# Optimization experiments

Measured on AMD Instinct MI355X. Metric: run time of the kernel, lower is better.

## Reference

```python
import jax, jax.numpy as jnp
import numpy as np

B, S, E, H = 4, 1024, 1024, 16
HD = E // H
EPS = 1e-10


def setup_inputs() -> dict:
    key = jax.random.key(0)
    ks = jax.random.split(key, 10)
    w = lambda k: jax.random.normal(k, (E, E), jnp.float32) * 0.02
    b = lambda k: jax.random.normal(k, (E,), jnp.float32) * 0.02
    return {
        "query": jax.random.normal(ks[0], (B, S, E), jnp.float32),
        "Wq": w(ks[1]), "bq": b(ks[2]),
        "Wk": w(ks[3]), "bk": b(ks[4]),
        "Wv": w(ks[5]), "bv": b(ks[6]),
        "Wo": w(ks[7]), "bo": b(ks[8]),
        "alpha": jnp.array(1.0, jnp.float32),
    }


def reference(query, Wq, bq, Wk, bk, Wv, bv, Wo, bo, alpha):
    scale = 1.0 / np.sqrt(HD)
    # projections -> [B, H, S, HD]
    def heads(x, W, bias):
        return (x @ W.T + bias).reshape(B, S, H, HD).transpose(0, 2, 1, 3)
    Q = heads(query, Wq, bq)
    K = heads(query, Wk, bk)
    V = heads(query, Wv, bv)
    # raw scores [B, H, S, S]
    scores = jnp.einsum('bhqd,bhkd->bhqk', Q, K) * scale
    # 2D FFT over the (q, k) plane
    scores_fft = jnp.fft.fft2(scores, axes=(-2, -1))
    # spectral filter: exp(i * alpha * arctan(log|F| + eps))
    phase = alpha * jnp.arctan(jnp.log(jnp.abs(scores_fft) + EPS))
    filt = jnp.exp(1j * phase)
    scores_filtered = jnp.fft.ifft2(scores_fft * filt, axes=(-2, -1)).real
    # softmax over keys (dropout is identity at eval)
    attn = jax.nn.softmax(scores_filtered, axis=-1)
    ctx = jnp.einsum('bhqk,bhkd->bhqd', attn, V)
    ctx = ctx.transpose(0, 2, 1, 3).reshape(B, S, E)
    return ctx @ Wo.T + bo
```

## Files before the change

kernel.cpp:

```cpp
#include <hip/hip_runtime.h>
#include <hip/hip_fp16.h>


typedef __attribute__((ext_vector_type(8))) short short8;
typedef __attribute__((ext_vector_type(8))) _Float16 half8;
typedef __attribute__((ext_vector_type(4))) float f32x4;

#define PITCH 40
#define PITCH1 72
#define TP 40

__device__ __forceinline__ float bf2f(short v) {
  return __uint_as_float(((unsigned)(unsigned short)v) << 16);
}
__device__ __forceinline__ short f2bf(float f) {
  unsigned u = __float_as_uint(f);
  u += 0x7FFFu + ((u >> 16) & 1u);
  return (short)(u >> 16);
}

__device__ __forceinline__ short8 ld8(const void* p, size_t idx, int isf32) {
  short8 r;
  if (isf32) {
    const float* f = (const float*)p + idx;
    float4 a = *(const float4*)f;
    float4 b = *(const float4*)(f + 4);
    r[0] = f2bf(a.x); r[1] = f2bf(a.y); r[2] = f2bf(a.z); r[3] = f2bf(a.w);
    r[4] = f2bf(b.x); r[5] = f2bf(b.y); r[6] = f2bf(b.z); r[7] = f2bf(b.w);
  } else {
    r = *(const short8*)((const short*)p + idx);
  }
  return r;
}
__device__ __forceinline__ float ldf(const void* p, int idx, int isf32) {
  return isf32 ? ((const float*)p)[idx] : bf2f(((const short*)p)[idx]);
}

__device__ __forceinline__ float2 cmul(float2 a, float2 b) {
  return make_float2(a.x * b.x - a.y * b.y, a.x * b.y + a.y * b.x);
}
__device__ __forceinline__ float2 cadd(float2 a, float2 b) {
  return make_float2(a.x + b.x, a.y + b.y);
}
__device__ __forceinline__ float2 csub(float2 a, float2 b) {
  return make_float2(a.x - b.x, a.y - b.y);
}
__device__ __forceinline__ half8 hneg(half8 v) {
  int4 t = *(int4*)&v;
  t.x ^= 0x80008000; t.y ^= 0x80008000; t.z ^= 0x80008000; t.w ^= 0x80008000;
  return *(half8*)&t;
}


template <int SGN>
__device__ __forceinline__ void dft16_dif(float2* x) {
  const float C16[8] = {1.f, 0.92387953f, 0.70710678f, 0.38268343f,
                        0.f, -0.38268343f, -0.70710678f, -0.92387953f};
  const float S16[8] = {0.f, 0.38268343f, 0.70710678f, 0.92387953f,
                        1.f, 0.92387953f, 0.70710678f, 0.38268343f};
#pragma unroll
  for (int h = 8; h >= 1; h >>= 1)
#pragma unroll
    for (int b = 0; b < 16; b += 2 * h)
#pragma unroll
      for (int i = 0; i < h; ++i) {
        const int e = i * (8 / h);
        float2 u = x[b + i], v = x[b + i + h];
        x[b + i] = cadd(u, v);
        float2 d = csub(u, v);
        float2 w = make_float2(C16[e], SGN > 0 ? S16[e] : -S16[e]);
        x[b + i + h] = (e == 0) ? d : cmul(d, w);
      }
}

template <int SGN>
__device__ __forceinline__ void midtw(float2* x, int lane) {
  const int rho[16] = {0, 8, 4, 12, 2, 10, 6, 14, 1, 9, 5, 13, 3, 11, 7, 15};
  float s, c;
  __sincosf((float)lane * 0.00613592315f, &s, &c);
  float2 w = make_float2(c, SGN > 0 ? s : -s);
  float2 run = w;
  x[8] = cmul(x[8], run);
#pragma unroll
  for (int e = 2; e < 16; ++e) {
    run = cmul(run, w);
    x[rho[e]] = cmul(x[rho[e]], run);
  }
}

template <int SGN>
__device__ __forceinline__ void xlane_dif(float2* x, int lane) {
#pragma unroll
  for (int h = 32; h >= 1; h >>= 1) {
    const int e = (lane & (h - 1)) * (32 / h);
    float s, c;
    __sincosf((float)e * 0.09817477042f, &s, &c);
    float2 w = make_float2(c, SGN > 0 ? s : -s);
    const bool hi = (lane & h) != 0;
#pragma unroll
    for (int r = 0; r < 16; ++r) {
      float2 t = x[r];
      float2 p;
      p.x = __shfl_xor(t.x, h, 64);
      p.y = __shfl_xor(t.y, h, 64);
      x[r] = hi ? cmul(csub(p, t), w) : cadd(t, p);
    }
  }
}

template <int SGN>
__device__ __forceinline__ void wfft1024_dif(float2* x, int lane) {
  dft16_dif<SGN>(x);
  midtw<SGN>(x, lane);
  xlane_dif<SGN>(x, lane);
}

template <int SGN>
__device__ __forceinline__ void midtw2(float2* x, float2* y, int lane) {
  const int rho[16] = {0, 8, 4, 12, 2, 10, 6, 14, 1, 9, 5, 13, 3, 11, 7, 15};
  float s, c;
  __sincosf((float)lane * 0.00613592315f, &s, &c);
  float2 w = make_float2(c, SGN > 0 ? s : -s);
  float2 run = w;
  x[8] = cmul(x[8], run);
  y[8] = cmul(y[8], run);
#pragma unroll
  for (int e = 2; e < 16; ++e) {
    run = cmul(run, w);
    x[rho[e]] = cmul(x[rho[e]], run);
    y[rho[e]] = cmul(y[rho[e]], run);
  }
}

template <int SGN>
__device__ __forceinline__ void xlane_dif2(float2* x, float2* y, int lane) {
#pragma unroll
  for (int h = 32; h >= 1; h >>= 1) {
    const int e = (lane & (h - 1)) * (32 / h);
    float s, c;
    __sincosf((float)e * 0.09817477042f, &s, &c);
    float2 w = make_float2(c, SGN > 0 ? s : -s);
    const bool hi = (lane & h) != 0;
#pragma unroll
    for (int r = 0; r < 16; ++r) {
      float2 t = x[r];
      float2 p;
      p.x = __shfl_xor(t.x, h, 64);
      p.y = __shfl_xor(t.y, h, 64);
      x[r] = hi ? cmul(csub(p, t), w) : cadd(t, p);
    }
#pragma unroll
    for (int r = 0; r < 16; ++r) {
      float2 t = y[r];
      float2 p;
      p.x = __shfl_xor(t.x, h, 64);
      p.y = __shfl_xor(t.y, h, 64);
      y[r] = hi ? cmul(csub(p, t), w) : cadd(t, p);
    }
  }
}

template <int SGN>
__device__ __forceinline__ void wfft1024_dif2(float2* x, float2* y, int lane) {
  dft16_dif<SGN>(x);
  dft16_dif<SGN>(y);
  midtw2<SGN>(x, y, lane);
  xlane_dif2<SGN>(x, y, lane);
}

__device__ __forceinline__ float gainw(float re, float im, float alpha, bool a1) {
  float mag2 = re * re + im * im;
  float t = 0.5f * __logf(mag2 + 1e-20f);
  if (a1) return __builtin_amdgcn_rsqf(fmaf(t, t, 1.0f)) * (1.0f / 1048576.0f);
  return __cosf(alpha * atanf(t)) * (1.0f / 1048576.0f);
}

__global__ void k0_detect(const unsigned* __restrict__ q,
                          const void* __restrict__ alphap, int* __restrict__ flags) {
  __shared__ float smax[256];
  __shared__ int szero[256];
  int t = threadIdx.x;
  float mx = 0.f; int zc = 0;
  for (int i = t; i < 16384; i += 256) {
    unsigned w = q[i];
    unsigned lo = w & 0xFFFFu;
    float v = fabsf(__uint_as_float(lo << 16));
    if (!(v <= 1e30f)) v = 1e30f;
    mx = fmaxf(mx, v);
    zc += (lo == 0u);
  }
  smax[t] = mx; szero[t] = zc;
  __syncthreads();
  for (int s = 128; s > 0; s >>= 1) {
    if (t < s) { smax[t] = fmaxf(smax[t], smax[t + s]); szero[t] += szero[t + s]; }
    __syncthreads();
  }
  if (t == 0) {
    int isf32 = (smax[0] > 100.f) || (szero[0] > 12288);
    flags[0] = isf32;
    float alpha = isf32 ? *(const float*)alphap : bf2f(*(const short*)alphap);
    ((float*)flags)[1] = alpha;
  }
}

__global__ __launch_bounds__(256) void k1_qkv(
    const void* __restrict__ x,
    const void* __restrict__ Wq, const void* __restrict__ bq,
    const void* __restrict__ Wk, const void* __restrict__ bk,
    const void* __restrict__ Wv, const void* __restrict__ bv,
    short* __restrict__ Qt, short* __restrict__ Kt, short* __restrict__ Vt,
    const int* __restrict__ flags)
{
  __shared__ __align__(16) char smem[128 * PITCH1 * 2 * 2];
  short* As = (short*)smem;
  short* Bs = As + 128 * PITCH1;
  short* Ct = (short*)smem;
  const int isf32 = flags[0];
  const int t = threadIdx.x;
  const int lb = blockIdx.x;
  const int m0 = ((lb & 7) * 4 + ((lb >> 3) & 3)) * 128;
  const int n0 = (lb >> 5) * 128;
  const int which = blockIdx.y;
  const void* __restrict__ W = (which == 0) ? Wq : (which == 1) ? Wk : Wv;
  const void* __restrict__ bias = (which == 0) ? bq : (which == 1) ? bk : bv;
  const int lane = t & 63, wvi = t >> 6;
  const int wr = wvi >> 1, wc = wvi & 1;
  const int lm = lane & 15, lq = lane >> 4;
  f32x4 acc[4][4] = {};

  for (int k0 = 0; k0 < 1024; k0 += 64) {
    __syncthreads();
#pragma unroll
    for (int i = 0; i < 4; ++i) {
      int l = t + i * 256;
      int row = l >> 3, kk = (l & 7) << 3;
      *(short8*)&As[row * PITCH1 + kk] = ld8(x, (size_t)(m0 + row) * 1024 + k0 + kk, isf32);
      *(short8*)&Bs[row * PITCH1 + kk] = ld8(W, (size_t)(n0 + row) * 1024 + k0 + kk, isf32);
    }
    __syncthreads();
#pragma unroll
    for (int kh = 0; kh < 2; ++kh) {
      short8 af[4], bf[4];
#pragma unroll
      for (int a = 0; a < 4; ++a)
        af[a] = *(const short8*)&As[(wr * 64 + a * 16 + lm) * PITCH1 + kh * 32 + lq * 8];
#pragma unroll
      for (int b = 0; b < 4; ++b)
        bf[b] = *(const short8*)&Bs[(wc * 64 + b * 16 + lm) * PITCH1 + kh * 32 + lq * 8];
#pragma unroll
      for (int a = 0; a < 4; ++a)
#pragma unroll
        for (int b = 0; b < 4; ++b)
          acc[a][b] = __builtin_amdgcn_mfma_f32_16x16x32_bf16(af[a], bf[b], acc[a][b], 0, 0, 0);
    }
  }

  __syncthreads();
#pragma unroll
  for (int a = 0; a < 4; ++a)
#pragma unroll
    for (int b = 0; b < 4; ++b) {
      int col = wc * 64 + b * 16 + lm;
      float bv_ = ldf(bias, n0 + col, isf32);
#pragma unroll
      for (int r = 0; r < 4; ++r) {
        int row = wr * 64 + a * 16 + lq * 4 + r;
        Ct[row * 136 + col] = f2bf(acc[a][b][r] + bv_);
      }
    }
  __syncthreads();

  short* __restrict__ O = (which == 0) ? Qt : (which == 1) ? Kt : Vt;
#pragma unroll
  for (int j = 0; j < 8; ++j) {
    int id = t + j * 256;
    int d128 = id & 127, sg = (id >> 7) * 8;
    short vals[8];
#pragma unroll
    for (int i = 0; i < 8; ++i) vals[i] = Ct[(sg + i) * 136 + d128];
    int col = n0 + d128;
    int h = col >> 6, d = col & 63;
    int bb = m0 >> 10, sbase = (m0 & 1023) + sg;
    *(short8*)&O[(((size_t)(bb * 16 + h)) << 16) + ((size_t)d << 10) + sbase] = *(short8*)vals;
  }
}

__global__ __launch_bounds__(128) void kA_qkfft(
    const short* __restrict__ Qt, const short* __restrict__ Kt,
    __half2* __restrict__ Qhat, __half2* __restrict__ Khat)
{
  __shared__ float2 sbuf[2][1024];
  const int lane = threadIdx.x & 63, w = threadIdx.x >> 6;
  const int z = blockIdx.y;
  const int bx = blockIdx.x;
  if (bx < 16) {
    const short* qp = Qt + ((size_t)z << 16);
    const int d0 = bx * 4 + w * 2;
    float2 x[16], y[16];
#pragma unroll
    for (int j = 0; j < 16; ++j) {
      x[j] = make_float2(0.125f * bf2f(qp[(d0 << 10) + lane + 64 * j]), 0.f);
      y[j] = make_float2(0.125f * bf2f(qp[((d0 + 1) << 10) + lane + 64 * j]), 0.f);
    }
    wfft1024_dif2<-1>(x, y, lane);
    __half2* o0 = Qhat + (((size_t)(z * 64 + d0)) << 10);
    __half2* o1 = o0 + 1024;
#pragma unroll
    for (int r = 0; r < 16; ++r) {
      o0[lane + 64 * r] = __float22half2_rn(x[r]);
      o1[lane + 64 * r] = __float22half2_rn(y[r]);
    }
  } else {
    const short* kp = Kt + ((size_t)z << 16);
    const int p = (bx - 16) * 2 + w;
    const int d0 = 2 * p;
    float2 x[16];
#pragma unroll
    for (int j = 0; j < 16; ++j)
      x[j] = make_float2(bf2f(kp[(d0 << 10) + lane + 64 * j]),
                         bf2f(kp[((d0 + 1) << 10) + lane + 64 * j]));
    wfft1024_dif<-1>(x, lane);
    const int rho[16] = {0, 8, 4, 12, 2, 10, 6, 14, 1, 9, 5, 13, 3, 11, 7, 15};
    const int bl6 = ((lane & 1) << 5) | ((lane & 2) << 3) | ((lane & 4) << 1) |
                    ((lane & 8) >> 1) | ((lane & 16) >> 3) | ((lane & 32) >> 5);
    float2* buf = sbuf[w];
#pragma unroll
    for (int r = 0; r < 16; ++r) buf[rho[r] + 16 * bl6] = x[r];
    __half2* o0 = Khat + (size_t)(z * 64 + d0) * 520;
    __half2* o1 = o0 + 520;
#pragma unroll 1
    for (int jj = 0; jj < 9; ++jj) {
      int v = lane + 64 * jj;
      if (v <= 512) {
        float2 A = buf[v], B = buf[(1024 - v) & 1023];
        o0[v] = __float22half2_rn(make_float2((A.x + B.x) * 0.5f, (A.y - B.y) * 0.5f));
        o1[v] = __float22half2_rn(make_float2((A.y + B.y) * 0.5f, (B.x - A.x) * 0.5f));
      }
    }
  }
}

__global__ __launch_bounds__(256) void kB_specmm(
    const __half2* __restrict__ Qhat, const __half2* __restrict__ Khat,
    __half2* __restrict__ Ct, const int* __restrict__ flags, int bh0)
{
  __shared__ unsigned short Are[64][72], Aim[64][72], Bre[128][72], Bim[128][72];
  const int t = threadIdx.x;
  const int u0 = blockIdx.x * 128;
  const int v0 = blockIdx.y * 64;
  const int zl = blockIdx.z;
  const int z = bh0 + zl;
  const float alpha = ((const float*)flags)[1];
  const bool a1 = (alpha == 1.0f);
  {
    const int d = t >> 2;
    const ushort2* src = (const ushort2*)(Khat + (size_t)(z * 64 + d) * 520);
    int vb = (t & 3) * 16;
#pragma unroll
    for (int j = 0; j < 16; ++j) {
      int v = v0 + vb + j;
      if (v > 519) v = 519;
      ushort2 e = src[v];
      int row = vb + j;
      int dc = d ^ (((row >> 4) & 3) << 4);
      Are[row][dc] = e.x;
      Aim[row][dc] = e.y;
    }
    const ushort2* srcb = (const ushort2*)(Qhat + (((size_t)(z * 64 + d)) << 10) + u0);
    int ub = (t & 3) * 32;
#pragma unroll
    for (int j = 0; j < 32; ++j) {
      ushort2 e = srcb[ub + j];
      int row = ub + j;
      int dc = d ^ (((row >> 5) & 3) << 4);
      Bre[row][dc] = e.x;
      Bim[row][dc] = e.y;
    }
  }
  __syncthreads();

  const int lane = t & 63, wc = t >> 6;
  const int lm = lane & 15, lq = lane >> 4;
  f32x4 cre[4][2] = {}, cim[4][2] = {};
#pragma unroll
  for (int ks = 0; ks < 2; ++ks) {
    half8 ar[4], ai[4], aiN[4], br[2], bi[2];
#pragma unroll
    for (int a = 0; a < 4; ++a) {
      int dc = (ks * 32 + lq * 8) ^ ((a & 3) << 4);
      ar[a] = *(const half8*)&Are[a * 16 + lm][dc];
      ai[a] = *(const half8*)&Aim[a * 16 + lm][dc];
      aiN[a] = hneg(ai[a]);
    }
#pragma unroll
    for (int n = 0; n < 2; ++n) {
      int dc = (ks * 32 + lq * 8) ^ ((wc & 3) << 4);
      br[n] = *(const half8*)&Bre[wc * 32 + n * 16 + lm][dc];
      bi[n] = *(const half8*)&Bim[wc * 32 + n * 16 + lm][dc];
    }
#pragma unroll
    for (int a = 0; a < 4; ++a)
#pragma unroll
      for (int n = 0; n < 2; ++n) {
        cre[a][n] = __builtin_amdgcn_mfma_f32_16x16x32_f16(ar[a], br[n], cre[a][n], 0, 0, 0);
        cre[a][n] = __builtin_amdgcn_mfma_f32_16x16x32_f16(aiN[a], bi[n], cre[a][n], 0, 0, 0);
        cim[a][n] = __builtin_amdgcn_mfma_f32_16x16x32_f16(ar[a], bi[n], cim[a][n], 0, 0, 0);
        cim[a][n] = __builtin_amdgcn_mfma_f32_16x16x32_f16(ai[a], br[n], cim[a][n], 0, 0, 0);
      }
  }

  __half2* outp = Ct + (size_t)zl * 513 * 1024 + u0 + wc * 32;
#pragma unroll
  for (int a = 0; a < 4; ++a)
#pragma unroll
    for (int r = 0; r < 4; ++r) {
      int v = v0 + a * 16 + lq * 4 + r;
      if (v < 513) {
#pragma unroll
        for (int n = 0; n < 2; ++n) {
          float re = cre[a][n][r], im = cim[a][n][r];
          float wf = gainw(re, im, alpha, a1);
          outp[(size_t)v * 1024 + n * 16 + lm] =
              __float22half2_rn(make_float2(re * wf, im * wf));
        }
      }
    }
}

__global__ __launch_bounds__(256) void k4_invfft(__half2* __restrict__ Ct, int nrows)
{
  __shared__ unsigned short CM[4][32][TP];
  __shared__ unsigned short SC[4][4][32][TP];
  const int tid = threadIdx.x;
  const int lane = tid & 63, w = tid >> 6;
  const int lm = lane & 15, lq = lane >> 4;

  for (int i = tid; i < 1024; i += 256) {
    int r = i >> 5, c = i & 31;
    int brc = ((c & 1) << 4) | ((c & 2) << 2) | (c & 4) | ((c & 8) >> 2) | ((c & 16) >> 4);
    float ang = (float)((brc * r) & 31) * 0.19634954084936207f;
    float sv, cv;
    __sincosf(ang, &sv, &cv);
    __half chh = __float2half(cv), shh = __float2half(sv);
    CM[0][r][c] = __half_as_ushort(chh);
    CM[1][r][c] = __half_as_ushort(__float2half(cv - __half2float(chh)));
    CM[2][r][c] = __half_as_ushort(shh);
    CM[3][r][c] = __half_as_ushort(__float2half(sv - __half2float(shh)));
  }
  __syncthreads();

  half8 cf[4][2];
#pragma unroll
  for (int cmp = 0; cmp < 4; ++cmp)
#pragma unroll
    for (int t = 0; t < 2; ++t)
      cf[cmp][t] = *(const half8*)&CM[cmp][t * 16 + lm][lq * 8];

  unsigned short (*MRE)[TP] = SC[w][0];
  unsigned short (*MIM)[TP] = SC[w][1];
  unsigned short (*TRE)[TP] = SC[w][2];
  unsigned short (*TIM)[TP] = SC[w][3];

  const int slot = blockIdx.x * 4 + w;
  __half2* __restrict__ plane = Ct + (size_t)blockIdx.y * 513 * 1024;

#pragma unroll 1
  for (int rr = 0; rr < 4; ++rr) {
    const int vrow = slot * 4 + rr;
    const bool act = (vrow < nrows);
    __half2* __restrict__ row = plane + ((size_t)(act ? vrow : 0) << 10);
    int4 ch4[4];
#pragma unroll
    for (int k = 0; k < 4; ++k)
      ch4[k] = act ? *(const int4*)&row[4 * (lane + 64 * k)] : make_int4(0, 0, 0, 0);
#pragma unroll
    for (int k = 0; k < 4; ++k) {
      const unsigned* e = (const unsigned*)&ch4[k];
      unsigned short re4[4], im4[4];
#pragma unroll
      for (int j = 0; j < 4; ++j) {
        unsigned u = e[j];
        re4[j] = (unsigned short)(u & 0xFFFFu);
        im4[j] = (unsigned short)((u >> 16) ^ 0x8000u);
      }
      int h = (lane >> 3) + 8 * k, c0 = 4 * (lane & 7);
      *(int2*)&MRE[h][c0] = *(int2*)re4;
      *(int2*)&MIM[h][c0] = *(int2*)im4;
    }
    __syncthreads();

    half8 mre[2], mng[2], mps[2];
#pragma unroll
    for (int t = 0; t < 2; ++t) {
      mre[t] = *(const half8*)&MRE[t * 16 + lm][lq * 8];
      mng[t] = *(const half8*)&MIM[t * 16 + lm][lq * 8];
      mps[t] = hneg(mng[t]);
    }
    f32x4 ar[2][2] = {}, ai[2][2] = {};
#pragma unroll
    for (int i = 0; i < 2; ++i)
#pragma unroll
      for (int j = 0; j < 2; ++j) {
        ar[i][j] = __builtin_amdgcn_mfma_f32_16x16x32_f16(mre[i], cf[0][j], ar[i][j], 0, 0, 0);
        ar[i][j] = __builtin_amdgcn_mfma_f32_16x16x32_f16(mre[i], cf[1][j], ar[i][j], 0, 0, 0);
        ar[i][j] = __builtin_amdgcn_mfma_f32_16x16x32_f16(mng[i], cf[2][j], ar[i][j], 0, 0, 0);
        ar[i][j] = __builtin_amdgcn_mfma_f32_16x16x32_f16(mng[i], cf[3][j], ar[i][j], 0, 0, 0);
        ai[i][j] = __builtin_amdgcn_mfma_f32_16x16x32_f16(mre[i], cf[2][j], ai[i][j], 0, 0, 0);
        ai[i][j] = __builtin_amdgcn_mfma_f32_16x16x32_f16(mre[i], cf[3][j], ai[i][j], 0, 0, 0);
        ai[i][j] = __builtin_amdgcn_mfma_f32_16x16x32_f16(mps[i], cf[0][j], ai[i][j], 0, 0, 0);
        ai[i][j] = __builtin_amdgcn_mfma_f32_16x16x32_f16(mps[i], cf[1][j], ai[i][j], 0, 0, 0);
      }

#pragma unroll
    for (int i = 0; i < 2; ++i)
#pragma unroll
      for (int j = 0; j < 2; ++j) {
        unsigned short tr4[4], ti4[4];
#pragma unroll
        for (int r = 0; r < 4; ++r) {
          int h = i * 16 + lq * 4 + r;
          int q0 = j * 16 + lm;
          int brh = ((h & 1) << 4) | ((h & 2) << 2) | (h & 4) | ((h & 8) >> 2) | ((h & 16) >> 4);
          float ang = (float)(brh * q0) * 0.006135923151542565f;
          float sv, cv;
          __sincosf(ang, &sv, &cv);
          float nre = ar[i][j][r], nim = ai[i][j][r];
          float tre = cv * nre - sv * nim;
          float tim = cv * nim + sv * nre;
          tr4[r] = __half_as_ushort(__float2half(tre));
          ti4[r] = __half_as_ushort(__float2half(-tim));
        }
        *(int2*)&TRE[j * 16 + lm][i * 16 + lq * 4] = *(int2*)tr4;
        *(int2*)&TIM[j * 16 + lm][i * 16 + lq * 4] = *(int2*)ti4;
      }
    __syncthreads();

    half8 tre[2], tng[2], tps[2];
#pragma unroll
    for (int t = 0; t < 2; ++t) {
      tre[t] = *(const half8*)&TRE[t * 16 + lm][lq * 8];
      tng[t] = *(const half8*)&TIM[t * 16 + lm][lq * 8];
      tps[t] = hneg(tng[t]);
    }
    f32x4 gr[2][2] = {}, gi[2][2] = {};
#pragma unroll
    for (int i = 0; i < 2; ++i)
#pragma unroll
      for (int j = 0; j < 2; ++j) {
        gr[i][j] = __builtin_amdgcn_mfma_f32_16x16x32_f16(cf[0][i], tre[j], gr[i][j], 0, 0, 0);
        gr[i][j] = __builtin_amdgcn_mfma_f32_16x16x32_f16(cf[1][i], tre[j], gr[i][j], 0, 0, 0);
        gr[i][j] = __builtin_amdgcn_mfma_f32_16x16x32_f16(cf[2][i], tng[j], gr[i][j], 0, 0, 0);
        gr[i][j] = __builtin_amdgcn_mfma_f32_16x16x32_f16(cf[3][i], tng[j], gr[i][j], 0, 0, 0);
        gi[i][j] = __builtin_amdgcn_mfma_f32_16x16x32_f16(cf[0][i], tps[j], gi[i][j], 0, 0, 0);
        gi[i][j] = __builtin_amdgcn_mfma_f32_16x16x32_f16(cf[1][i], tps[j], gi[i][j], 0, 0, 0);
        gi[i][j] = __builtin_amdgcn_mfma_f32_16x16x32_f16(cf[2][i], tre[j], gi[i][j], 0, 0, 0);
        gi[i][j] = __builtin_amdgcn_mfma_f32_16x16x32_f16(cf[3][i], tre[j], gi[i][j], 0, 0, 0);
      }

    if (act) {
#pragma unroll
      for (int i = 0; i < 2; ++i)
#pragma unroll
        for (int j = 0; j < 2; ++j)
#pragma unroll
          for (int r = 0; r < 4; ++r) {
            int q = 512 * i + 128 * lq + 32 * r + 16 * j + lm;
            row[q] = __float22half2_rn(make_float2(gr[i][j][r], gi[i][j][r]));
          }
    }
  }
}

__global__ __launch_bounds__(512) void k56_softmax_av(
    const __half2* __restrict__ Ct, const short* __restrict__ Vt,
    short* __restrict__ ctx, int bh0)
{
  __shared__ __align__(16) char GP[34816];
  const int tid = threadIdx.x;
  const int q0 = blockIdx.x * 16, z = blockIdx.y;
  const int lane = tid & 63, w = tid >> 6;
  const int lm = lane & 15, lq = lane >> 4;
  const __half2* __restrict__ in = Ct + (size_t)z * 513 * 1024;
#define GROW(m) ((__half2*)(GP + (m) * 2064))
  for (int id = tid; id < 2052; id += 512) {
    int v = id >> 2, qq = (id & 3) * 4;
    int4 o = *(const int4*)&in[(size_t)v * 1024 + q0 + qq];
    __half2* op = (__half2*)&o;
#pragma unroll
    for (int i = 0; i < 4; ++i) GROW(qq + i)[v] = op[i];
  }
  short* P = (short*)GP;
  const int bl6 = ((lane & 1) << 5) | ((lane & 2) << 3) | ((lane & 4) << 1) |
                  ((lane & 8) >> 1) | ((lane & 16) >> 3) | ((lane & 32) >> 5);
  __syncthreads();

  const int p = w;
  const __half2* g1 = GROW(2 * p);
  const __half2* g2 = GROW(2 * p + 1);
  float2 x[16];
#pragma unroll
  for (int j = 0; j < 16; ++j) {
    int v = lane + 64 * j;
    float2 a, b;
    if (v <= 512) {
      a = __half22float2(g1[v]);
      b = __half22float2(g2[v]);
    } else {
      int v2 = 1024 - v;
      float2 aa = __half22float2(g1[v2]), bb = __half22float2(g2[v2]);
      a = make_float2(aa.x, -aa.y);
      b = make_float2(bb.x, -bb.y);
    }
    x[j] = make_float2(a.x - b.y, a.y + b.x);
  }

  wfft1024_dif<1>(x, lane);

  float m1 = -3.4e38f, m2 = -3.4e38f;
#pragma unroll
  for (int j = 0; j < 16; ++j) { m1 = fmaxf(m1, x[j].x); m2 = fmaxf(m2, x[j].y); }
#pragma unroll
  for (int s = 32; s > 0; s >>= 1) {
    m1 = fmaxf(m1, __shfl_xor(m1, s, 64));
    m2 = fmaxf(m2, __shfl_xor(m2, s, 64));
  }
  float s1 = 0.f, s2 = 0.f;
#pragma unroll
  for (int j = 0; j < 16; ++j) {
    float e1 = __expf(x[j].x - m1), e2 = __expf(x[j].y - m2);
    x[j] = make_float2(e1, e2);
    s1 += e1; s2 += e2;
  }
#pragma unroll
  for (int s = 32; s > 0; s >>= 1) {
    s1 += __shfl_xor(s1, s, 64);
    s2 += __shfl_xor(s2, s, 64);
  }
  float inv1 = 1.0f / s1, inv2 = 1.0f / s2;

  __syncthreads();

  {
    const int rho[16] = {0, 8, 4, 12, 2, 10, 6, 14, 1, 9, 5, 13, 3, 11, 7, 15};
    short a0[16], a1[16];
#pragma unroll
    for (int pos = 0; pos < 16; ++pos) {
      const int j = rho[pos];
      a0[pos] = f2bf(x[j].x * inv1);
      a1[pos] = f2bf(x[j].y * inv2);
    }
    short* dst0 = &P[(2 * p) * 1040 + 16 * bl6];
    short* dst1 = &P[(2 * p + 1) * 1040 + 16 * bl6];
    *(short8*)dst0       = *(short8*)&a0[0];
    *(short8*)(dst0 + 8) = *(short8*)&a0[8];
    *(short8*)dst1       = *(short8*)&a1[0];
    *(short8*)(dst1 + 8) = *(short8*)&a1[8];
  }
  __syncthreads();

  const short* __restrict__ Vp = Vt + ((size_t)(bh0 + z) << 16);
  f32x4 acc[4] = {};
#pragma unroll
  for (int ks = 0; ks < 4; ++ks) {
    int k0 = w * 128 + ks * 32;
    short8 a0 = *(const short8*)&P[lm * 1040 + k0 + lq * 8];
#pragma unroll
    for (int b = 0; b < 4; ++b) {
      short8 bv = *(const short8*)&Vp[(size_t)(b * 16 + lm) * 1024 + k0 + lq * 8];
      acc[b] = __builtin_amdgcn_mfma_f32_16x16x32_bf16(a0, bv, acc[b], 0, 0, 0);
    }
  }
  __syncthreads();
  float* red = (float*)GP;
#pragma unroll
  for (int b = 0; b < 4; ++b)
#pragma unroll
    for (int r = 0; r < 4; ++r)
      red[(w * 16 + lq * 4 + r) * 68 + b * 16 + lm] = acc[b][r];
  __syncthreads();
  if (tid < 256) {
    int q = tid >> 4, d0 = (tid & 15) * 4;
    float s0 = 0.f, s1_ = 0.f, s2_ = 0.f, s3 = 0.f;
#pragma unroll
    for (int ww = 0; ww < 8; ++ww) {
      const float* rr = &red[(ww * 16 + q) * 68 + d0];
      s0 += rr[0]; s1_ += rr[1]; s2_ += rr[2]; s3 += rr[3];
    }
    short o4[4] = {f2bf(s0), f2bf(s1_), f2bf(s2_), f2bf(s3)};
    *(int2*)&ctx[(((size_t)(bh0 + z)) << 16) + (size_t)(q0 + q) * 64 + d0] = *(int2*)o4;
  }
#undef GROW
}

__global__ __launch_bounds__(256) void k7_out(
    const short* __restrict__ ctx, const void* __restrict__ Wo,
    const void* __restrict__ bo, void* __restrict__ out,
    const int* __restrict__ flags)
{
  __shared__ __align__(16) char smem[128 * 136 * 2];
  short* As = (short*)smem;
  short* Bs = As + 128 * PITCH;
  short* Ct = (short*)smem;
  const int isf32 = flags[0];
  const int t = threadIdx.x;
  const int lb = blockIdx.x;
  const int m0 = ((lb & 7) * 4 + ((lb >> 3) & 3)) * 128;
  const int n0 = (lb >> 5) * 128;
  const int lane = t & 63, wvi = t >> 6;
  const int wr = wvi >> 1, wc = wvi & 1;
  const int lm = lane & 15, lq = lane >> 4;
  f32x4 acc[4][4] = {};

  for (int k0 = 0; k0 < 1024; k0 += 32) {
    __syncthreads();
#pragma unroll
    for (int i = 0; i < 2; ++i) {
      int l = t + i * 256;
      int row = l >> 2, kk = (l & 3) << 3;
      int n = m0 + row, e = k0 + kk;
      size_t aaddr = (((size_t)((n >> 10) * 16 + (e >> 6))) << 16) + (size_t)((n & 1023) << 6) + (e & 63);
      *(int4*)&As[row * PITCH + kk] = *(const int4*)&ctx[aaddr];
      *(short8*)&Bs[row * PITCH + kk] = ld8(Wo, (size_t)(n0 + row) * 1024 + e, isf32);
    }
    __syncthreads();
    short8 af[4], bf[4];
#pragma unroll
    for (int a = 0; a < 4; ++a) af[a] = *(const short8*)&As[(wr * 64 + a * 16 + lm) * PITCH + lq * 8];
#pragma unroll
    for (int b = 0; b < 4; ++b) bf[b] = *(const short8*)&Bs[(wc * 64 + b * 16 + lm) * PITCH + lq * 8];
#pragma unroll
    for (int a = 0; a < 4; ++a)
#pragma unroll
      for (int b = 0; b < 4; ++b)
        acc[a][b] = __builtin_amdgcn_mfma_f32_16x16x32_bf16(af[a], bf[b], acc[a][b], 0, 0, 0);
  }

  if (isf32) {
#pragma unroll
    for (int a = 0; a < 4; ++a)
#pragma unroll
      for (int b = 0; b < 4; ++b) {
        int col = n0 + wc * 64 + b * 16 + lm;
        float bo_ = ldf(bo, col, 1);
#pragma unroll
        for (int r = 0; r < 4; ++r) {
          int row = m0 + wr * 64 + a * 16 + lq * 4 + r;
          ((float*)out)[(size_t)row * 1024 + col] = acc[a][b][r] + bo_;
        }
      }
    return;
  }
  __syncthreads();
#pragma unroll
  for (int a = 0; a < 4; ++a)
#pragma unroll
    for (int b = 0; b < 4; ++b) {
      int col = wc * 64 + b * 16 + lm;
      float bo_ = ldf(bo, n0 + col, 0);
#pragma unroll
      for (int r = 0; r < 4; ++r) {
        int row = wr * 64 + a * 16 + lq * 4 + r;
        Ct[row * 136 + col] = f2bf(acc[a][b][r] + bo_);
      }
    }
  __syncthreads();
#pragma unroll
  for (int j = 0; j < 8; ++j) {
    int id = t + j * 256;
    int row = id >> 4, c16 = (id & 15) * 8;
    short8 v = *(const short8*)&Ct[row * 136 + c16];
    *(short8*)&((short*)out)[(size_t)(m0 + row) * 1024 + n0 + c16] = v;
  }
}

extern "C" void kernel_launch(void* const* d_in, const int* in_sizes, int n_in,
                              void* d_out, int out_size, void* d_ws, size_t ws_size,
                              hipStream_t stream)
{
  const void* x  = d_in[0];
  const void* Wq = d_in[1];
  const void* bq = d_in[2];
  const void* Wk = d_in[3];
  const void* bk = d_in[4];
  const void* Wv = d_in[5];
  const void* bv = d_in[6];
  const void* Wo = d_in[7];
  const void* bo = d_in[8];
  const void* alphap = d_in[9];
  char* ws = (char*)d_ws;

  const size_t PLANE_CT = (size_t)513 * 1024 * 4;
  const size_t QH_SZ = (size_t)64 * 64 * 1024 * 4;
  const size_t KH_SZ = (size_t)64 * 64 * 520 * 4;

  const size_t B_CT  = 0;
  const size_t B_VT  = 64 * PLANE_CT;
  const size_t B_CX  = B_VT + ((size_t)8u << 20);
  const size_t B_QH  = B_CX + ((size_t)8u << 20);
  const size_t B_KH  = B_QH + QH_SZ;
  const size_t B_FL  = B_KH + KH_SZ;
  const size_t B_NEED = B_FL + 256;

  if (ws_size >= B_NEED) {
    short*   Qt   = (short*)(ws);
    short*   Kt   = (short*)(ws + ((size_t)8u << 20));
    short*   Vt   = (short*)(ws + B_VT);
    short*   ctx  = (short*)(ws + B_CX);
    __half2* Ct   = (__half2*)(ws + B_CT);
    __half2* Qhat = (__half2*)(ws + B_QH);
    __half2* Khat = (__half2*)(ws + B_KH);
    int*     flags = (int*)(ws + B_FL);

    k0_detect<<<1, 256, 0, stream>>>((const unsigned*)x, alphap, flags);
    k1_qkv<<<dim3(256, 3), 256, 0, stream>>>(x, Wq, bq, Wk, bk, Wv, bv, Qt, Kt, Vt, flags);
    kA_qkfft<<<dim3(32, 64), 128, 0, stream>>>(Qt, Kt, Qhat, Khat);
    kB_specmm<<<dim3(8, 9, 64), 256, 0, stream>>>(Qhat, Khat, Ct, flags, 0);
    k4_invfft<<<dim3(33, 64), 256, 0, stream>>>(Ct, 513);
    k56_softmax_av<<<dim3(64, 64), 512, 0, stream>>>(Ct, Vt, ctx, 0);
    k7_out<<<256, 256, 0, stream>>>(ctx, Wo, bo, d_out, flags);
    return;
  }

  const size_t VT_OFF = (size_t)17u << 20;
  const size_t CX_OFF = (size_t)25u << 20;
  const size_t QH_OFF = (size_t)33u << 20;
  const size_t KH_OFF = QH_OFF + QH_SZ;
  const size_t FL_OFF = KH_OFF + KH_SZ;

  short*   Qt   = (short*)(ws);
  short*   Kt   = (short*)(ws + ((size_t)8u << 20));
  short*   Vt   = (short*)(ws + VT_OFF);
  short*   ctx  = (short*)(ws + CX_OFF);
  __half2* Ct   = (__half2*)(ws);
  __half2* Qhat = (__half2*)(ws + QH_OFF);
  __half2* Khat = (__half2*)(ws + KH_OFF);
  int*     flags = (int*)(ws + FL_OFF);

  k0_detect<<<1, 256, 0, stream>>>((const unsigned*)x, alphap, flags);
  k1_qkv<<<dim3(256, 3), 256, 0, stream>>>(x, Wq, bq, Wk, bk, Wv, bv, Qt, Kt, Vt, flags);
  kA_qkfft<<<dim3(32, 64), 128, 0, stream>>>(Qt, Kt, Qhat, Khat);
  for (int c = 0; c < 8; ++c) {
    int bh0 = c * 8;
    kB_specmm<<<dim3(8, 9, 8), 256, 0, stream>>>(Qhat, Khat, Ct, flags, bh0);
    k4_invfft<<<dim3(33, 8), 256, 0, stream>>>(Ct, 513);
    k56_softmax_av<<<dim3(64, 8), 512, 0, stream>>>(Ct, Vt, ctx, bh0);
  }
  k7_out<<<256, 256, 0, stream>>>(ctx, Wo, bo, d_out, flags);
}
```

Baseline: 611.8 us.

## Replace per-row radix FFT in softmax kernel with MFMA 32x32 DFT decomposition

The 1024-point inverse FFT per row inside the softmax/AV kernel is replaced by a 32x32 Cooley-Tukey split. Both 32-point DFT stages run as f16 MFMA matrix products against a DFT twiddle matrix kept in shared memory, with an inter-stage twiddle multiply in between. The twiddle matrix is split into hi and lo halves to recover precision. This moves FFT arithmetic from scalar FMA work onto the matrix cores. In exchange it uses much more shared memory (about 75KB per block), which lowers occupancy, and it adds f16 rounding of intermediates plus per-block table setup.

```diff
diff --git a/kernel.cpp b/kernel.cpp
--- a/kernel.cpp
+++ b/kernel.cpp
@@ -50,7 +50,6 @@
   t.x ^= 0x80008000; t.y ^= 0x80008000; t.z ^= 0x80008000; t.w ^= 0x80008000;
   return *(half8*)&t;
 }
-
 
 template <int SGN>
 __device__ __forceinline__ void dft16_dif(float2* x) {
@@ -575,11 +574,35 @@
     const __half2* __restrict__ Ct, const short* __restrict__ Vt,
     short* __restrict__ ctx, int bh0)
 {
-  __shared__ __align__(16) char GP[34816];
+  __shared__ __align__(16) char GP[75776];
   const int tid = threadIdx.x;
   const int q0 = blockIdx.x * 16, z = blockIdx.y;
   const int lane = tid & 63, w = tid >> 6;
   const int lm = lane & 15, lq = lane >> 4;
+
+  {
+    unsigned short* CMf = (unsigned short*)GP;
+    for (int i = tid; i < 1024; i += 512) {
+      int r = i >> 5, c = i & 31;
+      float ang = (float)((r * c) & 31) * 0.19634954084936207f;
+      float sv, cv;
+      __sincosf(ang, &sv, &cv);
+      __half chh = __float2half(cv), shh = __float2half(sv);
+      CMf[0 * 32 * TP + r * TP + c] = __half_as_ushort(chh);
+      CMf[1 * 32 * TP + r * TP + c] = __half_as_ushort(__float2half(cv - __half2float(chh)));
+      CMf[2 * 32 * TP + r * TP + c] = __half_as_ushort(shh);
+      CMf[3 * 32 * TP + r * TP + c] = __half_as_ushort(__float2half(sv - __half2float(shh)));
+    }
+  }
+  __syncthreads();
+  half8 cf[4][2];
+#pragma unroll
+  for (int cmp = 0; cmp < 4; ++cmp)
+#pragma unroll
+    for (int t = 0; t < 2; ++t)
+      cf[cmp][t] = *(const half8*)&((unsigned short*)GP)[cmp * 32 * TP + (t * 16 + lm) * TP + lq * 8];
+  __syncthreads();
+
   const __half2* __restrict__ in = Ct + (size_t)z * 513 * 1024;
 #define GROW(m) ((__half2*)(GP + (m) * 2064))
   for (int id = tid; id < 2052; id += 512) {
@@ -589,36 +612,114 @@
 #pragma unroll
     for (int i = 0; i < 4; ++i) GROW(qq + i)[v] = op[i];
   }
-  short* P = (short*)GP;
-  const int bl6 = ((lane & 1) << 5) | ((lane & 2) << 3) | ((lane & 4) << 1) |
-                  ((lane & 8) >> 1) | ((lane & 16) >> 3) | ((lane & 32) >> 5);
-  __syncthreads();
-
-  const int p = w;
-  const __half2* g1 = GROW(2 * p);
-  const __half2* g2 = GROW(2 * p + 1);
-  float2 x[16];
-#pragma unroll
-  for (int j = 0; j < 16; ++j) {
-    int v = lane + 64 * j;
-    float2 a, b;
-    if (v <= 512) {
-      a = __half22float2(g1[v]);
-      b = __half22float2(g2[v]);
-    } else {
-      int v2 = 1024 - v;
-      float2 aa = __half22float2(g1[v2]), bb = __half22float2(g2[v2]);
-      a = make_float2(aa.x, -aa.y);
-      b = make_float2(bb.x, -bb.y);
-    }
-    x[j] = make_float2(a.x - b.y, a.y + b.x);
-  }
-
-  wfft1024_dif<1>(x, lane);
+  __syncthreads();
+
+  unsigned short (*SA)[TP] = (unsigned short (*)[TP])(GP + 34816 + w * 5120);
+  unsigned short (*SB)[TP] = (unsigned short (*)[TP])(GP + 34816 + w * 5120 + 2560);
+  {
+    const __half2* g1 = GROW(2 * w);
+    const __half2* g2 = GROW(2 * w + 1);
+    const int v0 = lane & 31;
+    const int v1b = (lane >> 5) * 16;
+    unsigned short re16[16], im16[16];
+#pragma unroll
+    for (int jj = 0; jj < 16; ++jj) {
+      int v = v0 + 32 * (v1b + jj);
+      float2 a, b;
+      if (v <= 512) {
+        a = __half22float2(g1[v]);
+        b = __half22float2(g2[v]);
+      } else {
+        int v2 = 1024 - v;
+        float2 aa = __half22float2(g1[v2]), bb = __half22float2(g2[v2]);
+        a = make_float2(aa.x, -aa.y);
+        b = make_float2(bb.x, -bb.y);
+      }
+      float zre = a.x - b.y, zim = a.y + b.x;
+      re16[jj] = __half_as_ushort(__float2half(zre));
+      im16[jj] = __half_as_ushort(__float2half(-zim));
+    }
+    *(short8*)&SA[v0][v1b]     = *(short8*)&re16[0];
+    *(short8*)&SA[v0][v1b + 8] = *(short8*)&re16[8];
+    *(short8*)&SB[v0][v1b]     = *(short8*)&im16[0];
+    *(short8*)&SB[v0][v1b + 8] = *(short8*)&im16[8];
+  }
+  __syncthreads();
+
+  half8 mre[2], mng[2], mps[2];
+#pragma unroll
+  for (int t = 0; t < 2; ++t) {
+    mre[t] = *(const half8*)&SA[t * 16 + lm][lq * 8];
+    mng[t] = *(const half8*)&SB[t * 16 + lm][lq * 8];
+    mps[t] = hneg(mng[t]);
+  }
+  f32x4 ar[2][2] = {}, ai[2][2] = {};
+#pragma unroll
+  for (int i = 0; i < 2; ++i)
+#pragma unroll
+    for (int j = 0; j < 2; ++j) {
+      ar[i][j] = __builtin_amdgcn_mfma_f32_16x16x32_f16(mre[i], cf[0][j], ar[i][j], 0, 0, 0);
+      ar[i][j] = __builtin_amdgcn_mfma_f32_16x16x32_f16(mre[i], cf[1][j], ar[i][j], 0, 0, 0);
+      ar[i][j] = __builtin_amdgcn_mfma_f32_16x16x32_f16(mng[i], cf[2][j], ar[i][j], 0, 0, 0);
+      ar[i][j] = __builtin_amdgcn_mfma_f32_16x16x32_f16(mng[i], cf[3][j], ar[i][j], 0, 0, 0);
+      ai[i][j] = __builtin_amdgcn_mfma_f32_16x16x32_f16(mre[i], cf[2][j], ai[i][j], 0, 0, 0);
+      ai[i][j] = __builtin_amdgcn_mfma_f32_16x16x32_f16(mre[i], cf[3][j], ai[i][j], 0, 0, 0);
+      ai[i][j] = __builtin_amdgcn_mfma_f32_16x16x32_f16(mps[i], cf[0][j], ai[i][j], 0, 0, 0);
+      ai[i][j] = __builtin_amdgcn_mfma_f32_16x16x32_f16(mps[i], cf[1][j], ai[i][j], 0, 0, 0);
+    }
+
+#pragma unroll
+  for (int i = 0; i < 2; ++i)
+#pragma unroll
+    for (int j = 0; j < 2; ++j) {
+      unsigned short tr4[4], ti4[4];
+#pragma unroll
+      for (int r = 0; r < 4; ++r) {
+        int v0 = i * 16 + lq * 4 + r;
+        int k0 = j * 16 + lm;
+        float ang = (float)(v0 * k0) * 0.006135923151542565f;
+        float sv, cv;
+        __sincosf(ang, &sv, &cv);
+        float nre = ar[i][j][r], nim = ai[i][j][r];
+        tr4[r] = __half_as_ushort(__float2half(cv * nre - sv * nim));
+        ti4[r] = __half_as_ushort(__float2half(-(cv * nim + sv * nre)));
+      }
+      *(int2*)&SA[j * 16 + lm][i * 16 + lq * 4] = *(int2*)tr4;
+      *(int2*)&SB[j * 16 + lm][i * 16 + lq * 4] = *(int2*)ti4;
+    }
+
+  half8 tre[2], tng[2], tps[2];
+#pragma unroll
+  for (int t = 0; t < 2; ++t) {
+    tre[t] = *(const half8*)&SA[t * 16 + lm][lq * 8];
+    tng[t] = *(const half8*)&SB[t * 16 + lm][lq * 8];
+    tps[t] = hneg(tng[t]);
+  }
+  f32x4 gr[2][2] = {}, gi[2][2] = {};
+#pragma unroll
+  for (int i = 0; i < 2; ++i)
+#pragma unroll
+    for (int j = 0; j < 2; ++j) {
+      gr[i][j] = __builtin_amdgcn_mfma_f32_16x16x32_f16(cf[0][i], tre[j], gr[i][j], 0, 0, 0);
+      gr[i][j] = __builtin_amdgcn_mfma_f32_16x16x32_f16(cf[1][i], tre[j], gr[i][j], 0, 0, 0);
+      gr[i][j] = __builtin_amdgcn_mfma_f32_16x16x32_f16(cf[2][i], tng[j], gr[i][j], 0, 0, 0);
+      gr[i][j] = __builtin_amdgcn_mfma_f32_16x16x32_f16(cf[3][i], tng[j], gr[i][j], 0, 0, 0);
+      gi[i][j] = __builtin_amdgcn_mfma_f32_16x16x32_f16(cf[0][i], tps[j], gi[i][j], 0, 0, 0);
+      gi[i][j] = __builtin_amdgcn_mfma_f32_16x16x32_f16(cf[1][i], tps[j], gi[i][j], 0, 0, 0);
+      gi[i][j] = __builtin_amdgcn_mfma_f32_16x16x32_f16(cf[2][i], tre[j], gi[i][j], 0, 0, 0);
+      gi[i][j] = __builtin_amdgcn_mfma_f32_16x16x32_f16(cf[3][i], tre[j], gi[i][j], 0, 0, 0);
+    }
 
   float m1 = -3.4e38f, m2 = -3.4e38f;
 #pragma unroll
-  for (int j = 0; j < 16; ++j) { m1 = fmaxf(m1, x[j].x); m2 = fmaxf(m2, x[j].y); }
+  for (int i = 0; i < 2; ++i)
+#pragma unroll
+    for (int j = 0; j < 2; ++j)
+#pragma unroll
+      for (int r = 0; r < 4; ++r) {
+        m1 = fmaxf(m1, gr[i][j][r]);
+        m2 = fmaxf(m2, gi[i][j][r]);
+      }
 #pragma unroll
   for (int s = 32; s > 0; s >>= 1) {
     m1 = fmaxf(m1, __shfl_xor(m1, s, 64));
@@ -626,11 +727,18 @@
   }
   float s1 = 0.f, s2 = 0.f;
 #pragma unroll
-  for (int j = 0; j < 16; ++j) {
-    float e1 = __expf(x[j].x - m1), e2 = __expf(x[j].y - m2);
-    x[j] = make_float2(e1, e2);
-    s1 += e1; s2 += e2;
-  }
+  for (int i = 0; i < 2; ++i)
+#pragma unroll
+    for (int j = 0; j < 2; ++j)
+#pragma unroll
+      for (int r = 0; r < 4; ++r) {
+        float e1 = __expf(gr[i][j][r] - m1);
+        float e2 = __expf(gi[i][j][r] - m2);
+        gr[i][j][r] = e1;
+        gi[i][j][r] = e2;
+        s1 += e1;
+        s2 += e2;
+      }
 #pragma unroll
   for (int s = 32; s > 0; s >>= 1) {
     s1 += __shfl_xor(s1, s, 64);
@@ -638,23 +746,28 @@
   }
   float inv1 = 1.0f / s1, inv2 = 1.0f / s2;
 
-  __syncthreads();
-
+  short* P = (short*)GP;
+#pragma unroll
+  for (int i = 0; i < 2; ++i)
+#pragma unroll
+    for (int j = 0; j < 2; ++j)
+#pragma unroll
+      for (int r = 0; r < 4; ++r) {
+        SA[i * 16 + lq * 4 + r][j * 16 + lm] = (unsigned short)f2bf(gr[i][j][r] * inv1);
+        SB[i * 16 + lq * 4 + r][j * 16 + lm] = (unsigned short)f2bf(gi[i][j][r] * inv2);
+      }
   {
-    const int rho[16] = {0, 8, 4, 12, 2, 10, 6, 14, 1, 9, 5, 13, 3, 11, 7, 15};
-    short a0[16], a1[16];
-#pragma unroll
-    for (int pos = 0; pos < 16; ++pos) {
-      const int j = rho[pos];
-      a0[pos] = f2bf(x[j].x * inv1);
-      a1[pos] = f2bf(x[j].y * inv2);
-    }
-    short* dst0 = &P[(2 * p) * 1040 + 16 * bl6];
-    short* dst1 = &P[(2 * p + 1) * 1040 + 16 * bl6];
-    *(short8*)dst0       = *(short8*)&a0[0];
-    *(short8*)(dst0 + 8) = *(short8*)&a0[8];
-    *(short8*)dst1       = *(short8*)&a1[0];
-    *(short8*)(dst1 + 8) = *(short8*)&a1[8];
+    int rowk = lane >> 1, colb = 16 * (lane & 1);
+    short8 a0 = *(short8*)&SA[rowk][colb];
+    short8 a1 = *(short8*)&SA[rowk][colb + 8];
+    short8 b0 = *(short8*)&SB[rowk][colb];
+    short8 b1 = *(short8*)&SB[rowk][colb + 8];
+    short* dst0 = &P[(2 * w) * 1040 + 16 * lane];
+    short* dst1 = &P[(2 * w + 1) * 1040 + 16 * lane];
+    *(short8*)dst0       = a0;
+    *(short8*)(dst0 + 8) = a1;
+    *(short8*)dst1       = b0;
+    *(short8*)(dst1 + 8) = b1;
   }
   __syncthreads();
 
```

Result: faster. 584.0 us (-4.5%).
